# Kernel tuning notes

Hardware: AMD Instinct MI355X
Metric: run time of the kernel (lower is better)

The kernel has to match this reference:

```python
import jax, jax.numpy as jnp
import numpy as np

N, F_IN, HEADS, F_OUT = 4096, 128, 4, 32
DENSITY = 0.05


def setup_inputs() -> dict:
    key = jax.random.key(0)
    k_x, k_adj, k_w, k_as, k_ad, k_b = jax.random.split(key, 6)
    x = jax.random.normal(k_x, (N, F_IN), dtype=jnp.float32)
    # binary adjacency with self-loops so every row of Tau_sum is nonzero
    adj = (jax.random.uniform(k_adj, (N, N)) < DENSITY).astype(jnp.float32)
    adj = jnp.maximum(adj, jnp.eye(N, dtype=jnp.float32))
    weight = jax.random.normal(k_w, (HEADS * F_OUT, F_IN), dtype=jnp.float32) * 0.1
    att_src = jax.random.normal(k_as, (1, HEADS, F_OUT), dtype=jnp.float32) * 0.1
    att_dst = jax.random.normal(k_ad, (1, HEADS, F_OUT), dtype=jnp.float32) * 0.1
    bias = jax.random.normal(k_b, (HEADS * F_OUT,), dtype=jnp.float32) * 0.1
    return {"x": x, "adj_matrix": adj, "weight": weight,
            "att_src": att_src, "att_dst": att_dst, "bias": bias}


def reference(x, adj_matrix, weight, att_src, att_dst, bias):
    n = x.shape[0]
    heads = att_src.shape[1]
    f_out = weight.shape[0] // heads
    # H' = x W^T, reshaped to [N, heads, F_out]
    h_prime = (x @ weight.T).reshape(n, heads, f_out)
    alpha_src = jnp.sum(h_prime * att_src, axis=-1)  # [N, heads]
    alpha_dst = jnp.sum(h_prime * att_dst, axis=-1)  # [N, heads]
    # C[m, n, h] = alpha_src[n, h] + alpha_dst[m, h]
    C = alpha_src[None, :, :] + alpha_dst[:, None, :]
    adj_t = adj_matrix.T[..., None]                  # [N, N, 1]
    # exp(leaky_relu(C, 0.2)) masked by adjacency
    tau = adj_t * jnp.exp(jnp.maximum(0.2 * C, C))   # [N, N, heads]
    tau_sum = jnp.sum(tau, axis=1, keepdims=True)    # [N, 1, heads]
    att_weights = tau / tau_sum
    # Z[m, h, f] = sum_n (adjT * att)[m, n, h] * H'[n, h, f]
    z = jnp.einsum('mnh,nhf->mhf', adj_t * att_weights, h_prime)
    return z.reshape(n, heads * f_out) + bias
```

## Files before the change

kernel.cpp:

```cpp
#include <hip/hip_runtime.h>
#include <hip/hip_bf16.h>

#define N_NODES 4096
#define F_IN    128
#define HEADS   4
#define FTOT    128
#define NSPLIT  8
#define NRANGE  (N_NODES / NSPLIT)
#define NSTEP   (NRANGE / 64)
#define HPB     512
#define BITB    1024
#define L2E     1.4426950408889634f

typedef __attribute__((ext_vector_type(8)))  short  short8v;
typedef __attribute__((ext_vector_type(16))) float  float16v;

static __device__ __forceinline__ unsigned f2bfu(float f) {
    union { __hip_bfloat16 h; unsigned short u; } cv;
    cv.h = __float2bfloat16(f);
    return (unsigned)cv.u;
}
static __device__ __forceinline__ unsigned cvt_pk_bf16(float lo, float hi) {
    unsigned r;
    asm("v_cvt_pk_bf16_f32 %0, %1, %2" : "=v"(r) : "v"(lo), "v"(hi));
    return r;
}

__global__ __launch_bounds__(256)
void k_pre(const float* __restrict__ x, const float* __restrict__ W,
           const float* __restrict__ att_src, const float* __restrict__ att_dst,
           const float* __restrict__ adj,
           unsigned short* __restrict__ hpt, float* __restrict__ ast,
           float* __restrict__ adt, unsigned* __restrict__ abits)
{
    const int t = threadIdx.x;
    if (blockIdx.x < HPB) {
        __shared__ alignas(16) float    xs[8 * F_IN];
        __shared__ alignas(16) unsigned hs[F_IN * 4];
        __shared__ float ssa[4][8], ssd[4][8];
        const int sub = t >> 7;
        const int tt  = t & 127;
        const int i0  = blockIdx.x * 8;
        reinterpret_cast<float4*>(xs)[t] =
            reinterpret_cast<const float4*>(x + (size_t)i0 * F_IN)[t];
        __syncthreads();

        const float4* W4  = reinterpret_cast<const float4*>(W + tt * F_IN);
        const float4* xs4 = reinterpret_cast<const float4*>(xs + sub * 4 * F_IN);
        float a0 = 0.f, a1 = 0.f, a2 = 0.f, a3 = 0.f;
#pragma unroll
        for (int k = 0; k < F_IN / 4; ++k) {
            const float4 w  = W4[k];
            const float4 v0 = xs4[k], v1 = xs4[32 + k], v2 = xs4[64 + k], v3 = xs4[96 + k];
            a0 = fmaf(w.x, v0.x, a0); a0 = fmaf(w.y, v0.y, a0); a0 = fmaf(w.z, v0.z, a0); a0 = fmaf(w.w, v0.w, a0);
            a1 = fmaf(w.x, v1.x, a1); a1 = fmaf(w.y, v1.y, a1); a1 = fmaf(w.z, v1.z, a1); a1 = fmaf(w.w, v1.w, a1);
            a2 = fmaf(w.x, v2.x, a2); a2 = fmaf(w.y, v2.y, a2); a2 = fmaf(w.z, v2.z, a2); a2 = fmaf(w.w, v2.w, a2);
            a3 = fmaf(w.x, v3.x, a3); a3 = fmaf(w.y, v3.y, a3); a3 = fmaf(w.z, v3.z, a3); a3 = fmaf(w.w, v3.w, a3);
        }
        hs[tt * 4 + sub * 2 + 0] = f2bfu(a0) | (f2bfu(a1) << 16);
        hs[tt * 4 + sub * 2 + 1] = f2bfu(a2) | (f2bfu(a3) << 16);

        const float asv = att_src[tt], adv = att_dst[tt];
        float s0 = a0 * asv, s1 = a1 * asv, s2 = a2 * asv, s3 = a3 * asv;
        float d0 = a0 * adv, d1 = a1 * adv, d2 = a2 * adv, d3 = a3 * adv;
#pragma unroll
        for (int s = 16; s; s >>= 1) {
            s0 += __shfl_xor(s0, s); s1 += __shfl_xor(s1, s);
            s2 += __shfl_xor(s2, s); s3 += __shfl_xor(s3, s);
            d0 += __shfl_xor(d0, s); d1 += __shfl_xor(d1, s);
            d2 += __shfl_xor(d2, s); d3 += __shfl_xor(d3, s);
        }
        if ((tt & 31) == 0) {
            const int hh = tt >> 5;
            ssa[hh][sub * 4 + 0] = s0 * L2E; ssa[hh][sub * 4 + 1] = s1 * L2E;
            ssa[hh][sub * 4 + 2] = s2 * L2E; ssa[hh][sub * 4 + 3] = s3 * L2E;
            ssd[hh][sub * 4 + 0] = d0 * L2E; ssd[hh][sub * 4 + 1] = d1 * L2E;
            ssd[hh][sub * 4 + 2] = d2 * L2E; ssd[hh][sub * 4 + 3] = d3 * L2E;
        }
        __syncthreads();
        if (t < 128)
            *reinterpret_cast<uint4*>(hpt + (size_t)t * N_NODES + i0) =
                *reinterpret_cast<const uint4*>(&hs[t * 4]);
        if (t < 64) {
            const int sd = t >> 5, hh = (t >> 3) & 3, nn = t & 7;
            const float v = sd ? ssd[hh][nn] : ssa[hh][nn];
            (sd ? adt : ast)[hh * N_NODES + i0 + nn] = v;
        }
    } else {
        __shared__ alignas(16) unsigned short lb[64 * 16];
        const int sblk  = blockIdx.x - HPB;
        const int strip = sblk & 63;
        const int chunk = sblk >> 6;
        const int c0    = strip * 64;
        const int r0    = chunk * 256;
        const int q     = t & 15;
        const int p     = t >> 4;
        const float4* adj4 = reinterpret_cast<const float4*>(adj);

        float4 v[16];
#pragma unroll
        for (int it = 0; it < 16; ++it)
            v[it] = adj4[(size_t)(r0 + p * 16 + it) * (N_NODES / 4) + (c0 >> 2) + q];
        unsigned mk0 = 0, mk1 = 0, mk2 = 0, mk3 = 0;
#pragma unroll
        for (int it = 0; it < 16; ++it) {
            mk0 |= (v[it].x != 0.f) ? (1u << it) : 0u;
            mk1 |= (v[it].y != 0.f) ? (1u << it) : 0u;
            mk2 |= (v[it].z != 0.f) ? (1u << it) : 0u;
            mk3 |= (v[it].w != 0.f) ? (1u << it) : 0u;
        }
        lb[(4 * q + 0) * 16 + p] = (unsigned short)mk0;
        lb[(4 * q + 1) * 16 + p] = (unsigned short)mk1;
        lb[(4 * q + 2) * 16 + p] = (unsigned short)mk2;
        lb[(4 * q + 3) * 16 + p] = (unsigned short)mk3;
        __syncthreads();
        const unsigned* lb32 = reinterpret_cast<const unsigned*>(lb);
#pragma unroll
        for (int j = 0; j < 2; ++j) {
            const int w = t + j * 256;
            const int m = w >> 3, col = w & 7;
            abits[(size_t)(c0 + m) * (N_NODES / 32) + chunk * 8 + col] = lb32[w];
        }
    }
}

__global__ __launch_bounds__(256, 4)
void k_main(const unsigned short* __restrict__ hpt, const float* __restrict__ ast,
            const float* __restrict__ adt, const unsigned* __restrict__ abits,
            float* __restrict__ z_part, float* __restrict__ taup)
{
    __shared__ alignas(16) float as_s[HEADS * NRANGE];
    const int t     = threadIdx.x;
    const int wv    = t >> 6;
    const int l     = t & 63;
    const int np    = l >> 5;
    const int lm    = l & 31;
    const int mt    = blockIdx.x >> 3;
    const int split = blockIdx.x & 7;
    const int m0    = mt * 32;
    const int nb0   = split * NRANGE;

    {
        const float4* src = reinterpret_cast<const float4*>(ast);
        float4* dst = reinterpret_cast<float4*>(as_s);
#pragma unroll
        for (int j = 0; j < 2; ++j) {
            const int lin = t * 2 + j;
            const int h   = lin >> 7;
            const int j4  = lin & 127;
            dst[lin] = src[h * (N_NODES / 4) + (nb0 >> 2) + j4];
        }
    }
    uint4 brow[4];
    {
        const uint4* bsrc = reinterpret_cast<const uint4*>(
            abits + (size_t)(m0 + lm) * (N_NODES / 32) + split * 16);
#pragma unroll
        for (int j = 0; j < 4; ++j) brow[j] = bsrc[j];
    }
    const float adm = adt[wv * N_NODES + m0 + lm];
    __syncthreads();

    const unsigned short* hrow = hpt + (size_t)(wv * 32 + lm) * N_NODES + nb0 + np * 8;
    const float* asw = as_s + wv * NRANGE;

    float16v acc, acct;
#pragma unroll
    for (int r = 0; r < 16; ++r) { acc[r] = 0.f; acct[r] = 0.f; }
    union { short8v v; unsigned u[4]; } ones;
#pragma unroll
    for (int j = 0; j < 4; ++j) ones.u[j] = 0x3F803F80u;

#pragma unroll
    for (int step = 0; step < NSTEP; ++step) {
#pragma unroll
        for (int q = 0; q < 4; ++q) {
            const short8v bv = *reinterpret_cast<const short8v*>(hrow + step * 64 + q * 16);
            const float4 a0 = *reinterpret_cast<const float4*>(asw + step * 64 + q * 16 + np * 8);
            const float4 a1 = *reinterpret_cast<const float4*>(asw + step * 64 + q * 16 + np * 8 + 4);
            const unsigned w32 = (&brow[0].x)[((2 * step + (q >> 1)) & 15)];
            const unsigned bb  = (w32 >> (((q & 1) << 4) + (np << 3))) & 0xFFu;
            auto wq = [&](float a, unsigned bit) {
                const float c  = a + adm;
                const float ex = exp2f(fmaxf(0.2f * c, c));
                return (bb & bit) ? ex : 0.f;
            };
            const float w0 = wq(a0.x, 1u),  w1 = wq(a0.y, 2u);
            const float w2 = wq(a0.z, 4u),  w3 = wq(a0.w, 8u);
            const float w4 = wq(a1.x, 16u), w5 = wq(a1.y, 32u);
            const float w6 = wq(a1.z, 64u), w7 = wq(a1.w, 128u);
            union { short8v v; unsigned u[4]; } af;
            af.u[0] = cvt_pk_bf16(w0, w1);
            af.u[1] = cvt_pk_bf16(w2, w3);
            af.u[2] = cvt_pk_bf16(w4, w5);
            af.u[3] = cvt_pk_bf16(w6, w7);
            acc  = __builtin_amdgcn_mfma_f32_32x32x16_bf16(af.v, bv, acc, 0, 0, 0);
            acct = __builtin_amdgcn_mfma_f32_32x32x16_bf16(af.v, ones.v, acct, 0, 0, 0);
        }
    }

    if (lm == 0) {
#pragma unroll
        for (int r = 0; r < 16; ++r) {
            const int row = (r & 3) + 8 * (r >> 2) + 4 * np;
            taup[((size_t)split * HEADS + wv) * N_NODES + m0 + row] = acct[r];
        }
    }
    float* zp = z_part + (size_t)split * N_NODES * FTOT;
#pragma unroll
    for (int r = 0; r < 16; ++r) {
        const int row = (r & 3) + 8 * (r >> 2) + 4 * np;
        zp[(size_t)(m0 + row) * FTOT + wv * 32 + lm] = acc[r];
    }
}

__global__ __launch_bounds__(256)
void k_fin(const float* __restrict__ z_part, const float* __restrict__ taup,
           const float* __restrict__ bias, float* __restrict__ out)
{
    const int idx = blockIdx.x * 256 + threadIdx.x;
    const int m = idx >> 5, f4 = idx & 31, h = f4 >> 3;
    const float4* zp4 = reinterpret_cast<const float4*>(z_part);
    float4 z = make_float4(0.f, 0.f, 0.f, 0.f);
    float ts = 0.f;
#pragma unroll
    for (int s = 0; s < NSPLIT; ++s) {
        const float4 zs = zp4[(size_t)s * N_NODES * (FTOT / 4) + idx];
        z.x += zs.x; z.y += zs.y; z.z += zs.z; z.w += zs.w;
        ts += taup[((size_t)s * HEADS + h) * N_NODES + m];
    }
    const float inv = 1.f / ts;
    const float4 b = reinterpret_cast<const float4*>(bias)[f4];
    float4 o;
    o.x = z.x * inv + b.x; o.y = z.y * inv + b.y;
    o.z = z.z * inv + b.z; o.w = z.w * inv + b.w;
    reinterpret_cast<float4*>(out)[idx] = o;
}

extern "C" void kernel_launch(void* const* d_in, const int* in_sizes, int n_in,
                              void* d_out, int out_size, void* d_ws, size_t ws_size,
                              hipStream_t stream) {
    const float* x       = (const float*)d_in[0];
    const float* adj     = (const float*)d_in[1];
    const float* weight  = (const float*)d_in[2];
    const float* att_src = (const float*)d_in[3];
    const float* att_dst = (const float*)d_in[4];
    const float* bias    = (const float*)d_in[5];
    float* out = (float*)d_out;

    unsigned short* hpt = (unsigned short*)d_ws;
    float* ast = (float*)(hpt + (size_t)FTOT * N_NODES);
    float* adt = ast + (size_t)HEADS * N_NODES;
    unsigned* abits = (unsigned*)(adt + (size_t)HEADS * N_NODES);
    float* z_part = (float*)(abits + (size_t)N_NODES * (N_NODES / 32));
    float* taup = z_part + (size_t)NSPLIT * N_NODES * FTOT;

    k_pre <<<HPB + BITB, 256, 0, stream>>>(x, weight, att_src, att_dst, adj,
                                           hpt, ast, adt, abits);
    k_main<<<(N_NODES / 32) * NSPLIT, 256, 0, stream>>>(hpt, ast, adt, abits,
                                                        z_part, taup);
    k_fin <<<N_NODES * (FTOT / 4) / 256, 256, 0, stream>>>(z_part, taup, bias, out);
}
```

Measured before the change: 54.30 us.

## Factor exp of leaky-relu into precomputed exponentials and prefetch H' tiles

The per-edge exp2(leaky_relu(a_src+a_dst)) is rewritten as a product of precomputed exponentials: exp2(a_src) and exp2(0.2*a_src) are computed once per source node into shared memory, and exp2(a_dst) and exp2(0.2*a_dst) once per destination row. The inner loop then needs only two multiplies and a select instead of an add, max and transcendental per edge. The loop also loads the next step's H' fragments into registers before the current step's MFMAs run. This costs twice the shared memory for the source terms and extra registers, and the factored form can overflow or lose precision for large logits.

```diff
diff --git a/kernel.cpp b/kernel.cpp
--- a/kernel.cpp
+++ b/kernel.cpp
@@ -129,7 +129,7 @@
             const float* __restrict__ adt, const unsigned* __restrict__ abits,
             float* __restrict__ z_part, float* __restrict__ taup)
 {
-    __shared__ alignas(16) float as_s[HEADS * NRANGE];
+    __shared__ alignas(16) float2 ea_s[HEADS * NRANGE];
     const int t     = threadIdx.x;
     const int wv    = t >> 6;
     const int l     = t & 63;
@@ -140,16 +140,14 @@
     const int m0    = mt * 32;
     const int nb0   = split * NRANGE;
 
-    {
-        const float4* src = reinterpret_cast<const float4*>(ast);
-        float4* dst = reinterpret_cast<float4*>(as_s);
-#pragma unroll
-        for (int j = 0; j < 2; ++j) {
-            const int lin = t * 2 + j;
-            const int h   = lin >> 7;
-            const int j4  = lin & 127;
-            dst[lin] = src[h * (N_NODES / 4) + (nb0 >> 2) + j4];
-        }
+#pragma unroll
+    for (int j = 0; j < 8; ++j) {
+        const int lin = j * 256 + t;
+        const int h   = lin >> 9;
+        const int n   = lin & 511;
+        const float a = ast[h * N_NODES + nb0 + n];
+        ea_s[lin] = make_float2(__builtin_amdgcn_exp2f(a),
+                                __builtin_amdgcn_exp2f(0.2f * a));
     }
     uint4 brow[4];
     {
@@ -159,10 +157,12 @@
         for (int j = 0; j < 4; ++j) brow[j] = bsrc[j];
     }
     const float adm = adt[wv * N_NODES + m0 + lm];
+    const float ed1 = __builtin_amdgcn_exp2f(adm);
+    const float ed2 = __builtin_amdgcn_exp2f(0.2f * adm);
     __syncthreads();
 
     const unsigned short* hrow = hpt + (size_t)(wv * 32 + lm) * N_NODES + nb0 + np * 8;
-    const float* asw = as_s + wv * NRANGE;
+    const float2* eaw = ea_s + wv * NRANGE;
 
     float16v acc, acct;
 #pragma unroll
@@ -171,32 +171,42 @@
 #pragma unroll
     for (int j = 0; j < 4; ++j) ones.u[j] = 0x3F803F80u;
 
+    short8v cur[4], nxt[4];
+#pragma unroll
+    for (int q = 0; q < 4; ++q)
+        cur[q] = *reinterpret_cast<const short8v*>(hrow + q * 16);
+
 #pragma unroll
     for (int step = 0; step < NSTEP; ++step) {
+        if (step + 1 < NSTEP) {
+#pragma unroll
+            for (int q = 0; q < 4; ++q)
+                nxt[q] = *reinterpret_cast<const short8v*>(hrow + (step + 1) * 64 + q * 16);
+        }
 #pragma unroll
         for (int q = 0; q < 4; ++q) {
-            const short8v bv = *reinterpret_cast<const short8v*>(hrow + step * 64 + q * 16);
-            const float4 a0 = *reinterpret_cast<const float4*>(asw + step * 64 + q * 16 + np * 8);
-            const float4 a1 = *reinterpret_cast<const float4*>(asw + step * 64 + q * 16 + np * 8 + 4);
+            const float2* eap = eaw + step * 64 + q * 16 + np * 8;
             const unsigned w32 = (&brow[0].x)[((2 * step + (q >> 1)) & 15)];
             const unsigned bb  = (w32 >> (((q & 1) << 4) + (np << 3))) & 0xFFu;
-            auto wq = [&](float a, unsigned bit) {
-                const float c  = a + adm;
-                const float ex = exp2f(fmaxf(0.2f * c, c));
-                return (bb & bit) ? ex : 0.f;
-            };
-            const float w0 = wq(a0.x, 1u),  w1 = wq(a0.y, 2u);
-            const float w2 = wq(a0.z, 4u),  w3 = wq(a0.w, 8u);
-            const float w4 = wq(a1.x, 16u), w5 = wq(a1.y, 32u);
-            const float w6 = wq(a1.z, 64u), w7 = wq(a1.w, 128u);
+            float w[8];
+#pragma unroll
+            for (int i = 0; i < 8; ++i) {
+                const float2 e = eap[i];
+                const float p1 = e.x * ed1;
+                const float p2 = e.y * ed2;
+                const float sel = (p1 > 1.0f) ? p1 : p2;
+                w[i] = (bb & (1u << i)) ? sel : 0.f;
+            }
             union { short8v v; unsigned u[4]; } af;
-            af.u[0] = cvt_pk_bf16(w0, w1);
-            af.u[1] = cvt_pk_bf16(w2, w3);
-            af.u[2] = cvt_pk_bf16(w4, w5);
-            af.u[3] = cvt_pk_bf16(w6, w7);
-            acc  = __builtin_amdgcn_mfma_f32_32x32x16_bf16(af.v, bv, acc, 0, 0, 0);
+            af.u[0] = cvt_pk_bf16(w[0], w[1]);
+            af.u[1] = cvt_pk_bf16(w[2], w[3]);
+            af.u[2] = cvt_pk_bf16(w[4], w[5]);
+            af.u[3] = cvt_pk_bf16(w[6], w[7]);
+            acc  = __builtin_amdgcn_mfma_f32_32x32x16_bf16(af.v, cur[q], acc, 0, 0, 0);
             acct = __builtin_amdgcn_mfma_f32_32x32x16_bf16(af.v, ones.v, acct, 0, 0, 0);
         }
+#pragma unroll
+        for (int q = 0; q < 4; ++q) cur[q] = nxt[q];
     }
 
     if (lm == 0) {
```

After: 47.18 us. 1.15x faster.
